# Optimization experiments

Hardware: AMD Instinct MI355X
Metric: run time of the kernel (lower is better)

The kernel has to match this reference:

```python
import jax, jax.numpy as jnp
import numpy as np

ALPHA = 1.702
LIMIT = 7.0
TOP_K = 4


def setup_inputs() -> dict:
    key = jax.random.key(0)
    ks = jax.random.split(key, 7)
    B, S, H, E, I = 2, 1024, 1024, 16, 2048
    scale_w = 1.0 / np.sqrt(H)
    return {
        "hidden_states": jax.random.normal(ks[0], (B, S, H), jnp.float32),
        "router_weight": jax.random.normal(ks[1], (E, H), jnp.float32) * scale_w,
        "router_bias": jax.random.normal(ks[2], (E,), jnp.float32) * 0.01,
        "gate_up_proj": jax.random.normal(ks[3], (E, H, 2 * I), jnp.float32) * scale_w,
        "gate_up_proj_bias": jax.random.normal(ks[4], (E, 2 * I), jnp.float32) * 0.01,
        "down_proj": jax.random.normal(ks[5], (E, I, H), jnp.float32) * (1.0 / np.sqrt(I)),
        "down_proj_bias": jax.random.normal(ks[6], (E, H), jnp.float32) * 0.01,
    }


def reference(hidden_states, router_weight, router_bias, gate_up_proj,
              gate_up_proj_bias, down_proj, down_proj_bias):
    B, S, H = hidden_states.shape
    E = router_weight.shape[0]
    dt = hidden_states.dtype

    # Router: linear -> softmax -> top-k -> renormalize
    router_logits = jnp.einsum('bsh,eh->bse', hidden_states, router_weight) + router_bias
    router_probs = jax.nn.softmax(router_logits, axis=-1)
    topk_weights, topk_indices = jax.lax.top_k(router_probs, TOP_K)  # [B,S,K]
    topk_weights = topk_weights / jnp.sum(topk_weights, axis=-1, keepdims=True)

    # Sparsity mask [B,S,E]: 1 for active experts (semantics of tt.sparse_matmul)
    onehot = jax.nn.one_hot(topk_indices, E, dtype=dt)        # [B,S,K,E]
    sparsity = jnp.sum(onehot, axis=2)                         # [B,S,E] (0/1)

    # Fused gate+up projection (interleaved layout), masked per-expert
    gate_up = jnp.einsum('bsh,ehf->bsef', hidden_states, gate_up_proj)  # [B,S,E,2I]
    gate_up = gate_up * sparsity[..., None]
    gate = gate_up[..., 0::2] + gate_up_proj_bias[:, 0::2]     # [B,S,E,I]
    up = gate_up[..., 1::2] + gate_up_proj_bias[:, 1::2]

    gate = jnp.minimum(gate, LIMIT)
    up = jnp.clip(up, -LIMIT, LIMIT)
    glu = gate * jax.nn.sigmoid(gate * ALPHA)
    activated = (up + 1.0) * glu                               # [B,S,E,I]

    # Down projection, masked per-expert, then bias
    down = jnp.einsum('bsei,eih->bseh', activated, down_proj)  # [B,S,E,H]
    down = down * sparsity[..., None] + down_proj_bias         # bias broadcasts [E,H]

    # Scatter top-k weights to full expert dim and combine
    full_weights = jnp.sum(onehot * topk_weights[..., None], axis=2)   # [B,S,E]
    output = jnp.sum(down * full_weights[..., None], axis=2)           # [B,S,H]
    return output, topk_weights
```

## Files before the change

### kernel.cpp

```cpp
#include <hip/hip_runtime.h>

#define TOKENS 2048
#define HD 1024
#define NEXP 16
#define TWO_I 4096
#define ID 2048

typedef short short8 __attribute__((ext_vector_type(8)));
typedef float f32x4 __attribute__((ext_vector_type(4)));
typedef unsigned short ushort;

static __device__ __forceinline__ ushort f2bf(float f) {
    union { float f; unsigned u; } v; v.f = f;
    unsigned r = v.u + 0x7FFFu + ((v.u >> 16) & 1u);
    return (ushort)(r >> 16);
}

static __device__ __forceinline__ void gload_lds16(const void* g, void* l) {
    __builtin_amdgcn_global_load_lds(
        (const __attribute__((address_space(1))) unsigned int*)(g),
        (__attribute__((address_space(3))) unsigned int*)(l), 16, 0, 0);
}

__global__ __launch_bounds__(256) void cvt_kernel(const float* __restrict__ hs,
                                                  ushort* __restrict__ hb) {
    int i = (blockIdx.x * 256 + threadIdx.x) * 4;
    float4 v = *(const float4*)(hs + i);
    union { ushort b[4]; float2 f2; } u;
    u.b[0] = f2bf(v.x); u.b[1] = f2bf(v.y); u.b[2] = f2bf(v.z); u.b[3] = f2bf(v.w);
    *(float2*)(hb + i) = u.f2;
}

__global__ __launch_bounds__(256) void transpose_cvt_kernel(
    const float* __restrict__ src, ushort* __restrict__ dst, int K, int N) {
    const int e = blockIdx.z;
    const int n0 = blockIdx.x * 64;
    const int k0 = blockIdx.y * 64;
    __shared__ float T[64][68];
    const float* s = src + (size_t)e * K * N + (size_t)k0 * N + n0;
    const int r = threadIdx.x >> 4;
    const int c4 = (threadIdx.x & 15) * 4;
#pragma unroll
    for (int i = 0; i < 64; i += 16) {
        float4 v = *(const float4*)(s + (size_t)(r + i) * N + c4);
        T[r + i][c4 + 0] = v.x; T[r + i][c4 + 1] = v.y;
        T[r + i][c4 + 2] = v.z; T[r + i][c4 + 3] = v.w;
    }
    __syncthreads();
    const int n = threadIdx.x >> 2;
    const int kc = (threadIdx.x & 3) * 16;
    union { ushort b[16]; short8 v[2]; } o;
#pragma unroll
    for (int j = 0; j < 16; ++j) o.b[j] = f2bf(T[kc + j][n]);
    ushort* d = dst + (size_t)e * N * K + (size_t)(n0 + n) * K + k0 + kc;
    *(short8*)(d) = o.v[0];
    *(short8*)(d + 8) = o.v[1];
}

__global__ __launch_bounds__(256) void router_kernel(
    const float* __restrict__ hs, const float* __restrict__ rw,
    const float* __restrict__ rb, float* __restrict__ topk_w_out,
    int* __restrict__ topk_idx, int* __restrict__ counts) {
    const int wave = threadIdx.x >> 6;
    const int lane = threadIdx.x & 63;
    const int t = blockIdx.x * 4 + wave;

    float h[16];
#pragma unroll
    for (int j = 0; j < 16; ++j) h[j] = hs[t * HD + j * 64 + lane];

    __shared__ float lg[4][NEXP];
#pragma unroll
    for (int e = 0; e < NEXP; ++e) {
        float acc = 0.f;
#pragma unroll
        for (int j = 0; j < 16; ++j) acc += h[j] * rw[e * HD + j * 64 + lane];
#pragma unroll
        for (int s = 32; s > 0; s >>= 1) acc += __shfl_xor(acc, s);
        if (lane == 0) lg[wave][e] = acc + rb[e];
    }
    if (lane == 0) {
        float mx = lg[wave][0];
        for (int e = 1; e < NEXP; ++e) mx = fmaxf(mx, lg[wave][e]);
        float pr[NEXP];
        for (int e = 0; e < NEXP; ++e) pr[e] = __expf(lg[wave][e] - mx);
        int idx[4]; float wv[4]; float sum4 = 0.f;
        for (int k = 0; k < 4; ++k) {
            int bi = 0; float bv = -1.f;
            for (int e = 0; e < NEXP; ++e)
                if (pr[e] > bv) { bv = pr[e]; bi = e; }
            idx[k] = bi; wv[k] = bv; pr[bi] = -2.f; sum4 += bv;
        }
        for (int k = 0; k < 4; ++k) {
            topk_w_out[t * 4 + k] = wv[k] / sum4;
            topk_idx[t * 4 + k] = idx[k];
            atomicAdd(&counts[idx[k]], 1);
        }
    }
}

__global__ void scan_kernel(const int* __restrict__ counts, int* __restrict__ offsets,
                            int* __restrict__ cursor) {
    if (threadIdx.x == 0 && blockIdx.x == 0) {
        int o = 0;
        for (int e = 0; e < NEXP; ++e) { offsets[e] = o; cursor[e] = o; o += counts[e]; }
        offsets[NEXP] = o;
    }
}

__global__ __launch_bounds__(256) void build_kernel(
    const int* __restrict__ topk_idx, const float* __restrict__ topk_w,
    int* __restrict__ cursor, int* __restrict__ token_list, float* __restrict__ slot_w,
    int* __restrict__ slot_of) {
    int t = blockIdx.x * 256 + threadIdx.x;
    for (int k = 0; k < 4; ++k) {
        int e = topk_idx[t * 4 + k];
        int pos = atomicAdd(&cursor[e], 1);
        token_list[pos] = t;
        slot_w[pos] = topk_w[t * 4 + k];
        slot_of[t * 4 + k] = pos;
    }
}


__global__ __launch_bounds__(256) void gemm1_t_kernel(
    const ushort* __restrict__ hb, const ushort* __restrict__ gupT,
    const float* __restrict__ gub, const int* __restrict__ offsets,
    const int* __restrict__ token_list, ushort* __restrict__ act) {
    const int e = blockIdx.z;
    const int so = offsets[e];
    const int ne = offsets[e + 1] - so;
    const int row0 = blockIdx.y * 128;
    if (row0 >= ne) return;
    const int n0 = blockIdx.x * 128;

    __shared__ ushort As[2][4096];
    __shared__ ushort Bs[2][4096];

    const int tid = threadIdx.x;
    const int lane = tid & 63;
    const int w = tid >> 6;
    const int m = lane & 15;
    const int q = lane >> 4;
    const int wm = (w >> 1) * 64;
    const int wn = (w & 1) * 64;

    const int r0 = tid >> 2;
    const int ce = (tid & 3) * 8;
    int ar0 = row0 + r0;       if (ar0 >= ne) ar0 = ne - 1;
    int ar1 = row0 + 64 + r0;  if (ar1 >= ne) ar1 = ne - 1;
    const ushort* ga0 = hb + (size_t)token_list[so + ar0] * HD + ce;
    const ushort* ga1 = hb + (size_t)token_list[so + ar1] * HD + ce;
    const ushort* gb0 = gupT + (size_t)e * TWO_I * HD + (size_t)(n0 + r0) * HD + ce;
    const ushort* gb1 = gb0 + (size_t)64 * HD;

    f32x4 acc[4][4] = {};

#define STAGE1(B, K0) do { \
    gload_lds16(ga0 + (K0), As[B] + w * 512); \
    gload_lds16(ga1 + (K0), As[B] + 2048 + w * 512); \
    gload_lds16(gb0 + (K0), Bs[B] + w * 512); \
    gload_lds16(gb1 + (K0), Bs[B] + 2048 + w * 512); \
} while (0)

#define COMPUTE1(B) do { \
    short8 af[4], bfr[4]; \
    _Pragma("unroll") for (int rt = 0; rt < 4; ++rt) \
        af[rt] = *(const short8*)(As[B] + (wm + rt * 16 + m) * 32 + q * 8); \
    _Pragma("unroll") for (int c = 0; c < 4; ++c) \
        bfr[c] = *(const short8*)(Bs[B] + (wn + c * 16 + m) * 32 + q * 8); \
    _Pragma("unroll") for (int rt = 0; rt < 4; ++rt) \
        _Pragma("unroll") for (int c = 0; c < 4; ++c) \
            acc[rt][c] = __builtin_amdgcn_mfma_f32_16x16x32_bf16(af[rt], bfr[c], acc[rt][c], 0, 0, 0); \
} while (0)

    STAGE1(0, 0);
    asm volatile("s_waitcnt vmcnt(0)" ::: "memory");
    __syncthreads();
    int cur = 0;
    for (int k0 = 32; k0 < HD; k0 += 32) {
        STAGE1(cur ^ 1, k0);
        COMPUTE1(cur);
        asm volatile("s_waitcnt vmcnt(0)" ::: "memory");
        __syncthreads();
        cur ^= 1;
    }
    COMPUTE1(cur);

#pragma unroll
    for (int c = 0; c < 4; ++c) {
        const int n = n0 + wn + c * 16 + m;
        const float bias = gub[e * TWO_I + n];
#pragma unroll
        for (int rt = 0; rt < 4; ++rt) {
#pragma unroll
            for (int rr = 0; rr < 4; ++rr) {
                const int grow = row0 + wm + rt * 16 + q * 4 + rr;
                float v = acc[rt][c][rr] + bias;
                float pv = __shfl_xor(v, 1);
                float gate = (m & 1) ? pv : v;
                float up   = (m & 1) ? v : pv;
                gate = fminf(gate, 7.0f);
                up = fminf(fmaxf(up, -7.0f), 7.0f);
                float glu = gate / (1.0f + __expf(-1.702f * gate));
                float a = (up + 1.0f) * glu;
                if (!(m & 1) && grow < ne)
                    act[(size_t)(so + grow) * ID + (n >> 1)] = f2bf(a);
            }
        }
    }
}

__global__ __launch_bounds__(256) void gemm2_t_kernel(
    const ushort* __restrict__ act, const ushort* __restrict__ downT,
    const int* __restrict__ offsets, float* __restrict__ dslot) {
    const int e = blockIdx.z;
    const int so = offsets[e];
    const int ne = offsets[e + 1] - so;
    const int row0 = blockIdx.y * 128;
    if (row0 >= ne) return;
    const int n0 = blockIdx.x * 128;

    __shared__ ushort As[2][4096];
    __shared__ ushort Bs[2][4096];

    const int tid = threadIdx.x;
    const int lane = tid & 63;
    const int w = tid >> 6;
    const int m = lane & 15;
    const int q = lane >> 4;
    const int wm = (w >> 1) * 64;
    const int wn = (w & 1) * 64;

    const int r0 = tid >> 2;
    const int ce = (tid & 3) * 8;
    const ushort* ga0 = act + (size_t)(so + row0 + r0) * ID + ce;
    const ushort* ga1 = ga0 + (size_t)64 * ID;
    const ushort* gb0 = downT + (size_t)e * HD * ID + (size_t)(n0 + r0) * ID + ce;
    const ushort* gb1 = gb0 + (size_t)64 * ID;

    f32x4 acc[4][4] = {};

#define STAGE2(B, K0) do { \
    gload_lds16(ga0 + (K0), As[B] + w * 512); \
    gload_lds16(ga1 + (K0), As[B] + 2048 + w * 512); \
    gload_lds16(gb0 + (K0), Bs[B] + w * 512); \
    gload_lds16(gb1 + (K0), Bs[B] + 2048 + w * 512); \
} while (0)

#define COMPUTE2(B) do { \
    short8 af[4], bfr[4]; \
    _Pragma("unroll") for (int rt = 0; rt < 4; ++rt) \
        af[rt] = *(const short8*)(As[B] + (wm + rt * 16 + m) * 32 + q * 8); \
    _Pragma("unroll") for (int c = 0; c < 4; ++c) \
        bfr[c] = *(const short8*)(Bs[B] + (wn + c * 16 + m) * 32 + q * 8); \
    _Pragma("unroll") for (int rt = 0; rt < 4; ++rt) \
        _Pragma("unroll") for (int c = 0; c < 4; ++c) \
            acc[rt][c] = __builtin_amdgcn_mfma_f32_16x16x32_bf16(af[rt], bfr[c], acc[rt][c], 0, 0, 0); \
} while (0)

    STAGE2(0, 0);
    asm volatile("s_waitcnt vmcnt(0)" ::: "memory");
    __syncthreads();
    int cur = 0;
    for (int k0 = 32; k0 < ID; k0 += 32) {
        STAGE2(cur ^ 1, k0);
        COMPUTE2(cur);
        asm volatile("s_waitcnt vmcnt(0)" ::: "memory");
        __syncthreads();
        cur ^= 1;
    }
    COMPUTE2(cur);

#pragma unroll
    for (int rt = 0; rt < 4; ++rt) {
#pragma unroll
        for (int rr = 0; rr < 4; ++rr) {
            const int grow = row0 + wm + rt * 16 + q * 4 + rr;
            if (grow < ne) {
                float* dp = dslot + (size_t)(so + grow) * HD + n0 + wn + m;
#pragma unroll
                for (int c = 0; c < 4; ++c) dp[c * 16] = acc[rt][c][rr];
            }
        }
    }
}

__global__ __launch_bounds__(256) void combine_kernel(
    const float* __restrict__ dslot, const float* __restrict__ dwb,
    const int* __restrict__ topk_idx, const int* __restrict__ slot_of,
    const float* __restrict__ topk_w, float* __restrict__ out) {
    const int t = blockIdx.x;
    const int n = threadIdx.x * 4;
    float4 o = {0.f, 0.f, 0.f, 0.f};
#pragma unroll
    for (int k = 0; k < 4; ++k) {
        const int e = topk_idx[t * 4 + k];
        const int s = slot_of[t * 4 + k];
        const float wgt = topk_w[t * 4 + k];
        float4 d = *(const float4*)(dslot + (size_t)s * HD + n);
        float4 b = *(const float4*)(dwb + (size_t)e * HD + n);
        o.x += wgt * (d.x + b.x);
        o.y += wgt * (d.y + b.y);
        o.z += wgt * (d.z + b.z);
        o.w += wgt * (d.w + b.w);
    }
    *(float4*)(out + (size_t)t * HD + n) = o;
}


__global__ __launch_bounds__(256) void gemm1_fb_kernel(
    const ushort* __restrict__ hb, const float* __restrict__ gup,
    const float* __restrict__ gub, const int* __restrict__ offsets,
    const int* __restrict__ token_list, ushort* __restrict__ act) {
    const int e = blockIdx.z;
    const int so = offsets[e];
    const int ne = offsets[e + 1] - so;
    const int row0 = blockIdx.y * 64;
    if (row0 >= ne) return;
    const int n0 = blockIdx.x * 64;
    __shared__ ushort Al[64][40];
    __shared__ ushort Bt[64][40];
    const int tid = threadIdx.x;
    const int lane = tid & 63;
    const int wave = tid >> 6;
    const int m = lane & 15;
    const int q = lane >> 4;
    const int ar = tid >> 2;
    const int ac = (tid & 3) * 8;
    int arow = row0 + ar; if (arow >= ne) arow = ne - 1;
    const int tok = token_list[so + arow];
    const ushort* aptr = hb + tok * HD + ac;
    const int bk = tid >> 3;
    const int bn = (tid & 7) * 8;
    const float* bptr = gup + (size_t)e * HD * TWO_I + (size_t)bk * TWO_I + n0 + bn;
    f32x4 acc[4] = {{0,0,0,0},{0,0,0,0},{0,0,0,0},{0,0,0,0}};
    for (int k0 = 0; k0 < HD; k0 += 32) {
        float4 av = *(const float4*)(aptr + k0);
        *(float4*)(&Al[ar][ac]) = av;
        const float* bp = bptr + (size_t)k0 * TWO_I;
        float4 b0 = *(const float4*)(bp);
        float4 b1 = *(const float4*)(bp + 4);
        Bt[bn + 0][bk] = f2bf(b0.x); Bt[bn + 1][bk] = f2bf(b0.y);
        Bt[bn + 2][bk] = f2bf(b0.z); Bt[bn + 3][bk] = f2bf(b0.w);
        Bt[bn + 4][bk] = f2bf(b1.x); Bt[bn + 5][bk] = f2bf(b1.y);
        Bt[bn + 6][bk] = f2bf(b1.z); Bt[bn + 7][bk] = f2bf(b1.w);
        __syncthreads();
        short8 af = *(const short8*)(&Al[wave * 16 + m][q * 8]);
#pragma unroll
        for (int c = 0; c < 4; ++c) {
            short8 bf = *(const short8*)(&Bt[c * 16 + m][q * 8]);
            acc[c] = __builtin_amdgcn_mfma_f32_16x16x32_bf16(af, bf, acc[c], 0, 0, 0);
        }
        __syncthreads();
    }
#pragma unroll
    for (int c = 0; c < 4; ++c) {
        const int n = n0 + c * 16 + m;
        const float bias = gub[e * TWO_I + n];
#pragma unroll
        for (int r = 0; r < 4; ++r) {
            const int grow = row0 + wave * 16 + q * 4 + r;
            float v = acc[c][r] + bias;
            float pv = __shfl_xor(v, 1);
            float gate = (m & 1) ? pv : v;
            float up   = (m & 1) ? v : pv;
            gate = fminf(gate, 7.0f);
            up = fminf(fmaxf(up, -7.0f), 7.0f);
            float glu = gate / (1.0f + __expf(-1.702f * gate));
            float a = (up + 1.0f) * glu;
            if (!(m & 1) && grow < ne)
                act[(size_t)(so + grow) * ID + (n >> 1)] = f2bf(a);
        }
    }
}

__global__ __launch_bounds__(256) void gemm2_fb_kernel(
    const ushort* __restrict__ act, const float* __restrict__ dwp,
    const float* __restrict__ dwb, const int* __restrict__ offsets,
    const int* __restrict__ token_list, const float* __restrict__ slot_w,
    float* __restrict__ out) {
    const int e = blockIdx.z;
    const int so = offsets[e];
    const int ne = offsets[e + 1] - so;
    const int row0 = blockIdx.y * 64;
    if (row0 >= ne) return;
    const int n0 = blockIdx.x * 64;
    __shared__ ushort Al[64][40];
    __shared__ ushort Bt[64][40];
    const int tid = threadIdx.x;
    const int lane = tid & 63;
    const int wave = tid >> 6;
    const int m = lane & 15;
    const int q = lane >> 4;
    const int ar = tid >> 2;
    const int ac = (tid & 3) * 8;
    int arow = row0 + ar; if (arow >= ne) arow = ne - 1;
    const ushort* aptr = act + (size_t)(so + arow) * ID + ac;
    const int bk = tid >> 3;
    const int bn = (tid & 7) * 8;
    const float* bptr = dwp + (size_t)e * ID * HD + (size_t)bk * HD + n0 + bn;
    f32x4 acc[4] = {{0,0,0,0},{0,0,0,0},{0,0,0,0},{0,0,0,0}};
    for (int k0 = 0; k0 < ID; k0 += 32) {
        float4 av = *(const float4*)(aptr + k0);
        *(float4*)(&Al[ar][ac]) = av;
        const float* bp = bptr + (size_t)k0 * HD;
        float4 b0 = *(const float4*)(bp);
        float4 b1 = *(const float4*)(bp + 4);
        Bt[bn + 0][bk] = f2bf(b0.x); Bt[bn + 1][bk] = f2bf(b0.y);
        Bt[bn + 2][bk] = f2bf(b0.z); Bt[bn + 3][bk] = f2bf(b0.w);
        Bt[bn + 4][bk] = f2bf(b1.x); Bt[bn + 5][bk] = f2bf(b1.y);
        Bt[bn + 6][bk] = f2bf(b1.z); Bt[bn + 7][bk] = f2bf(b1.w);
        __syncthreads();
        short8 af = *(const short8*)(&Al[wave * 16 + m][q * 8]);
#pragma unroll
        for (int c = 0; c < 4; ++c) {
            short8 bf = *(const short8*)(&Bt[c * 16 + m][q * 8]);
            acc[c] = __builtin_amdgcn_mfma_f32_16x16x32_bf16(af, bf, acc[c], 0, 0, 0);
        }
        __syncthreads();
    }
#pragma unroll
    for (int r = 0; r < 4; ++r) {
        const int grow = row0 + wave * 16 + q * 4 + r;
        if (grow < ne) {
            const int slot = so + grow;
            const int tok = token_list[slot];
            const float wgt = slot_w[slot];
#pragma unroll
            for (int c = 0; c < 4; ++c) {
                const int n = n0 + c * 16 + m;
                atomicAdd(&out[tok * HD + n], (acc[c][r] + dwb[e * HD + n]) * wgt);
            }
        }
    }
}

extern "C" void kernel_launch(void* const* d_in, const int* in_sizes, int n_in,
                              void* d_out, int out_size, void* d_ws, size_t ws_size,
                              hipStream_t stream) {
    const float* hs  = (const float*)d_in[0];
    const float* rw  = (const float*)d_in[1];
    const float* rb  = (const float*)d_in[2];
    const float* gup = (const float*)d_in[3];
    const float* gub = (const float*)d_in[4];
    const float* dwp = (const float*)d_in[5];
    const float* dwb = (const float*)d_in[6];

    float* out = (float*)d_out;
    float* topk_w = out + (size_t)TOKENS * HD;

    char* w = (char*)d_ws;
    int* counts     = (int*)(w + 0);
    int* cursor     = (int*)(w + 64);
    int* offsets    = (int*)(w + 128);
    int* token_list = (int*)(w + 256);
    float* slot_w   = (float*)(w + 256 + 32768);
    int* topk_idx   = (int*)(w + 256 + 65536);
    int* slot_of    = (int*)(w + 256 + 98304);
    ushort* hb      = (ushort*)(w + ((size_t)1 << 20));
    ushort* act     = (ushort*)(w + ((size_t)6 << 20));
    ushort* gupT    = (ushort*)(w + ((size_t)41 << 20));
    ushort* downT   = (ushort*)(w + ((size_t)169 << 20));
    float* dslot    = (float*)(w + ((size_t)233 << 20));
    const size_t need = (size_t)266 << 20;

    hipMemsetAsync(w, 0, 256, stream);

    cvt_kernel<<<2048, 256, 0, stream>>>(hs, hb);
    router_kernel<<<512, 256, 0, stream>>>(hs, rw, rb, topk_w, topk_idx, counts);
    scan_kernel<<<1, 64, 0, stream>>>(counts, offsets, cursor);
    build_kernel<<<8, 256, 0, stream>>>(topk_idx, topk_w, cursor, token_list, slot_w, slot_of);

    if (ws_size >= need) {
        transpose_cvt_kernel<<<dim3(TWO_I / 64, HD / 64, NEXP), 256, 0, stream>>>(
            gup, gupT, HD, TWO_I);
        transpose_cvt_kernel<<<dim3(HD / 64, ID / 64, NEXP), 256, 0, stream>>>(
            dwp, downT, ID, HD);
        gemm1_t_kernel<<<dim3(TWO_I / 128, TOKENS / 128, NEXP), 256, 0, stream>>>(
            hb, gupT, gub, offsets, token_list, act);
        gemm2_t_kernel<<<dim3(HD / 128, TOKENS / 128, NEXP), 256, 0, stream>>>(
            act, downT, offsets, dslot);
        combine_kernel<<<TOKENS, 256, 0, stream>>>(dslot, dwb, topk_idx, slot_of, topk_w, out);
    } else {
        hipMemsetAsync(out, 0, (size_t)TOKENS * HD * sizeof(float), stream);
        gemm1_fb_kernel<<<dim3(TWO_I / 64, TOKENS / 64, NEXP), 256, 0, stream>>>(
            hb, gup, gub, offsets, token_list, act);
        gemm2_fb_kernel<<<dim3(HD / 64, TOKENS / 64, NEXP), 256, 0, stream>>>(
            act, dwp, dwb, offsets, token_list, slot_w, out);
    }
}
```

Before: 842.7 us.

## Swizzle LDS tiles and restructure GEMM pipeline with partial waitcnt and priority

Both expert GEMM kernels now apply an XOR swizzle to the K-chunk column when loading global data into LDS and when reading MFMA fragments, to reduce LDS bank conflicts. The main loop is reordered so the next stage's loads are issued first, then the wave waits only for the older batch (vmcnt(4)) before a barrier, letting the prefetch overlap the compute. Compute is wrapped in s_setprio to favour MFMA issue. The change relies on the vmcnt counting being exact, and the raw s_barrier without a full waitcnt must still order LDS writes correctly.

After: 848.1 us. No clear change (+0.6%).

```diff
diff --git a/kernel.cpp b/kernel.cpp
--- a/kernel.cpp
+++ b/kernel.cpp
@@ -144,9 +144,10 @@
     const int q = lane >> 4;
     const int wm = (w >> 1) * 64;
     const int wn = (w & 1) * 64;
+    const int qa = (q ^ (m & 3)) * 8;
 
     const int r0 = tid >> 2;
-    const int ce = (tid & 3) * 8;
+    const int ce = (((tid & 3) ^ (r0 & 3)) * 8);
     int ar0 = row0 + r0;       if (ar0 >= ne) ar0 = ne - 1;
     int ar1 = row0 + 64 + r0;  if (ar1 >= ne) ar1 = ne - 1;
     const ushort* ga0 = hb + (size_t)token_list[so + ar0] * HD + ce;
@@ -166,25 +167,28 @@
 #define COMPUTE1(B) do { \
     short8 af[4], bfr[4]; \
     _Pragma("unroll") for (int rt = 0; rt < 4; ++rt) \
-        af[rt] = *(const short8*)(As[B] + (wm + rt * 16 + m) * 32 + q * 8); \
+        af[rt] = *(const short8*)(As[B] + (wm + rt * 16 + m) * 32 + qa); \
     _Pragma("unroll") for (int c = 0; c < 4; ++c) \
-        bfr[c] = *(const short8*)(Bs[B] + (wn + c * 16 + m) * 32 + q * 8); \
+        bfr[c] = *(const short8*)(Bs[B] + (wn + c * 16 + m) * 32 + qa); \
     _Pragma("unroll") for (int rt = 0; rt < 4; ++rt) \
         _Pragma("unroll") for (int c = 0; c < 4; ++c) \
             acc[rt][c] = __builtin_amdgcn_mfma_f32_16x16x32_bf16(af[rt], bfr[c], acc[rt][c], 0, 0, 0); \
 } while (0)
 
     STAGE1(0, 0);
+    int cur = 0;
+    for (int t = 0; t < HD / 32 - 1; ++t) {
+        STAGE1(cur ^ 1, (t + 1) * 32);
+        asm volatile("s_waitcnt vmcnt(4)" ::: "memory");
+        __builtin_amdgcn_s_barrier();
+        __builtin_amdgcn_s_setprio(1);
+        COMPUTE1(cur);
+        __builtin_amdgcn_s_setprio(0);
+        __builtin_amdgcn_s_barrier();
+        cur ^= 1;
+    }
     asm volatile("s_waitcnt vmcnt(0)" ::: "memory");
-    __syncthreads();
-    int cur = 0;
-    for (int k0 = 32; k0 < HD; k0 += 32) {
-        STAGE1(cur ^ 1, k0);
-        COMPUTE1(cur);
-        asm volatile("s_waitcnt vmcnt(0)" ::: "memory");
-        __syncthreads();
-        cur ^= 1;
-    }
+    __builtin_amdgcn_s_barrier();
     COMPUTE1(cur);
 
 #pragma unroll
@@ -231,9 +235,10 @@
     const int q = lane >> 4;
     const int wm = (w >> 1) * 64;
     const int wn = (w & 1) * 64;
+    const int qa = (q ^ (m & 3)) * 8;
 
     const int r0 = tid >> 2;
-    const int ce = (tid & 3) * 8;
+    const int ce = (((tid & 3) ^ (r0 & 3)) * 8);
     const ushort* ga0 = act + (size_t)(so + row0 + r0) * ID + ce;
     const ushort* ga1 = ga0 + (size_t)64 * ID;
     const ushort* gb0 = downT + (size_t)e * HD * ID + (size_t)(n0 + r0) * ID + ce;
@@ -251,25 +256,28 @@
 #define COMPUTE2(B) do { \
     short8 af[4], bfr[4]; \
     _Pragma("unroll") for (int rt = 0; rt < 4; ++rt) \
-        af[rt] = *(const short8*)(As[B] + (wm + rt * 16 + m) * 32 + q * 8); \
+        af[rt] = *(const short8*)(As[B] + (wm + rt * 16 + m) * 32 + qa); \
     _Pragma("unroll") for (int c = 0; c < 4; ++c) \
-        bfr[c] = *(const short8*)(Bs[B] + (wn + c * 16 + m) * 32 + q * 8); \
+        bfr[c] = *(const short8*)(Bs[B] + (wn + c * 16 + m) * 32 + qa); \
     _Pragma("unroll") for (int rt = 0; rt < 4; ++rt) \
         _Pragma("unroll") for (int c = 0; c < 4; ++c) \
             acc[rt][c] = __builtin_amdgcn_mfma_f32_16x16x32_bf16(af[rt], bfr[c], acc[rt][c], 0, 0, 0); \
 } while (0)
 
     STAGE2(0, 0);
+    int cur = 0;
+    for (int t = 0; t < ID / 32 - 1; ++t) {
+        STAGE2(cur ^ 1, (t + 1) * 32);
+        asm volatile("s_waitcnt vmcnt(4)" ::: "memory");
+        __builtin_amdgcn_s_barrier();
+        __builtin_amdgcn_s_setprio(1);
+        COMPUTE2(cur);
+        __builtin_amdgcn_s_setprio(0);
+        __builtin_amdgcn_s_barrier();
+        cur ^= 1;
+    }
     asm volatile("s_waitcnt vmcnt(0)" ::: "memory");
-    __syncthreads();
-    int cur = 0;
-    for (int k0 = 32; k0 < ID; k0 += 32) {
-        STAGE2(cur ^ 1, k0);
-        COMPUTE2(cur);
-        asm volatile("s_waitcnt vmcnt(0)" ::: "memory");
-        __syncthreads();
-        cur ^= 1;
-    }
+    __builtin_amdgcn_s_barrier();
     COMPUTE2(cur);
 
 #pragma unroll
```
